# Optimization experiments

Hardware: AMD Instinct MI355X
Metric: run time of the kernel (lower is better)

Reference implementation:

```python
import jax, jax.numpy as jnp
import numpy as np

B, N, C = 2, 65536, 256
HEADS, DIM_HEAD, SLICE_NUM = 8, 64, 64
INNER = HEADS * DIM_HEAD


def setup_inputs() -> dict:
    key = jax.random.key(0)
    ks = jax.random.split(key, 7)
    s_in = 1.0 / np.sqrt(C)
    s_dh = 1.0 / np.sqrt(DIM_HEAD)
    return {
        "x": jax.random.normal(ks[0], (B, N, C), dtype=jnp.float32),
        "Wx": jax.random.uniform(ks[1], (C, INNER), jnp.float32, -s_in, s_in),
        "bx": jax.random.uniform(ks[2], (INNER,), jnp.float32, -s_in, s_in),
        "Wfx": jax.random.uniform(ks[3], (C, INNER), jnp.float32, -s_in, s_in),
        "bfx": jax.random.uniform(ks[4], (INNER,), jnp.float32, -s_in, s_in),
        "Wslice": jax.random.uniform(ks[5], (DIM_HEAD, SLICE_NUM), jnp.float32, -s_dh, s_dh),
        "bslice": jax.random.uniform(ks[6], (SLICE_NUM,), jnp.float32, -s_dh, s_dh),
        "temperature": jnp.ones((1, HEADS, 1, 1), dtype=jnp.float32) * 0.5,
    }


def reference(x, Wx, bx, Wfx, bfx, Wslice, bslice, temperature):
    b, n, _ = x.shape
    # Linear projections, split heads: (B, N, H*D) -> (B, H, N, D)
    px = (x @ Wx + bx).reshape(b, n, HEADS, DIM_HEAD).transpose(0, 2, 1, 3)
    fx = (x @ Wfx + bfx).reshape(b, n, HEADS, DIM_HEAD).transpose(0, 2, 1, 3)
    # Project onto slices: (B, H, N, S)
    slice_proj = px @ Wslice + bslice
    # Temperature-scaled softmax over slices
    temp = jnp.clip(temperature, 0.5, 5.0)
    slice_weights = jax.nn.softmax(slice_proj / temp, axis=-1)
    # Normalize by per-slice mass over tokens, then aggregate
    slice_norm = slice_weights.sum(axis=2)  # (B, H, S)
    normed = slice_weights / (slice_norm[:, :, None, :] + 0.01)
    slice_tokens = jnp.einsum("bhns,bhnd->bhsd", normed, fx)
    return slice_tokens
```

## Files before the change

kernel.cpp:

```cpp
#include <hip/hip_runtime.h>
#include <hip/hip_bf16.h>


typedef __attribute__((ext_vector_type(8))) short short8;
typedef __attribute__((ext_vector_type(4))) short short4v;
typedef __attribute__((ext_vector_type(4))) float float4v;

#define WPITCH 264
#define TPITCH 72

__device__ __forceinline__ unsigned short f2bf(float f) {
    union { float f; unsigned int u; } v; v.f = f;
    unsigned int r = (v.u + 0x7FFFu + ((v.u >> 16) & 1u)) >> 16;
    return (unsigned short)r;
}

__global__ void msfe_prep(const float* __restrict__ Wx, const float* __restrict__ bx,
                          const float* __restrict__ Wfx,
                          const float* __restrict__ Wslice, const float* __restrict__ bslice,
                          unsigned short* __restrict__ Wt, float* __restrict__ bc) {
    int j = blockIdx.x;
    int c = threadIdx.x;
    if (j < 512) {
        int h = j >> 6, s = j & 63;
        float acc = 0.f;
        #pragma unroll 8
        for (int d = 0; d < 64; ++d)
            acc += Wx[c * 512 + h * 64 + d] * Wslice[d * 64 + s];
        Wt[j * 256 + c] = f2bf(acc);
        if (c == 0) {
            float b = bslice[s];
            for (int d = 0; d < 64; ++d) b += bx[h * 64 + d] * Wslice[d * 64 + s];
            bc[j] = b;
        }
    } else {
        int col = j - 512;
        Wt[j * 256 + c] = f2bf(Wfx[c * 512 + col]);
    }
}

__global__ __launch_bounds__(512, 2)
void msfe_main(const float* __restrict__ x,
               const unsigned short* __restrict__ Wt,
               const float* __restrict__ bc,
               const float* __restrict__ bfx,
               const float* __restrict__ temperature,
               float* __restrict__ Tg, float* __restrict__ ng) {
    __shared__ unsigned short Ws[128 * WPITCH];
    __shared__ unsigned short Xs[64 * WPITCH];
    __shared__ unsigned short wT[64 * TPITCH];
    __shared__ unsigned short fT[64 * TPITCH];

    const int tid  = threadIdx.x;
    const int lane = tid & 63;
    const int wv   = tid >> 6;
    const int quad = lane >> 4;
    const int l16  = lane & 15;

    const int bidx = blockIdx.x;
    const int c8   = bidx & 7;
    const int ti   = (bidx >> 3) & 3;
    const int head = (bidx >> 5) & 7;
    const int rnd  = bidx >> 8;
    const int tile = rnd * 32 + c8 * 4 + ti;
    const int batch = tile >> 7;
    const long tok0 = (long)tile * 512;

    {
        int r = tid & 127;
        int part = tid >> 7;
        int grow = (r < 64) ? (head * 64 + r) : (512 + head * 64 + (r - 64));
        const short4v* src = (const short4v*)(Wt + grow * 256 + part * 64);
        short4v* dst = (short4v*)(Ws + r * WPITCH + part * 64);
        #pragma unroll
        for (int j = 0; j < 16; ++j) dst[j] = src[j];
    }

    {
        const float4v* xg = (const float4v*)(x + tok0 * 256);
        #pragma unroll
        for (int i = 0; i < 8; ++i) {
            float4v v = xg[tid + i * 512];
            int f = (tid + i * 512) * 4;
            int trow = f >> 8, col = f & 255;
            short4v p;
            p.x = (short)f2bf(v.x); p.y = (short)f2bf(v.y);
            p.z = (short)f2bf(v.z); p.w = (short)f2bf(v.w);
            *(short4v*)(Xs + trow * WPITCH + col) = p;
        }
    }

    float bcr[4], bfxr[4];
    #pragma unroll
    for (int nt = 0; nt < 4; ++nt) {
        bcr[nt]  = bc [head * 64 + nt * 16 + l16];
        bfxr[nt] = bfx[head * 64 + nt * 16 + l16];
    }
    float tmp = temperature[head];
    tmp = fminf(fmaxf(tmp, 0.5f), 5.0f);
    const float invt = 1.0f / tmp;

    float4v Tac[2];
    Tac[0] = (float4v){0.f, 0.f, 0.f, 0.f};
    Tac[1] = (float4v){0.f, 0.f, 0.f, 0.f};
    float normAcc[4] = {0.f, 0.f, 0.f, 0.f};

    const int proj = wv >> 2;
    const int tw   = wv & 3;
    const int sh   = wv & 3;
    const int dh   = wv >> 2;

    __syncthreads();

    for (int c = 0; c < 8; ++c) {
        float4v xr[8];
        if (c < 7) {
            const float4v* xg = (const float4v*)(x + (tok0 + (long)(c + 1) * 64) * 256);
            #pragma unroll
            for (int i = 0; i < 8; ++i) xr[i] = xg[tid + i * 512];
        }

        float4v acc[4];
        #pragma unroll
        for (int nt = 0; nt < 4; ++nt) acc[nt] = (float4v){0.f, 0.f, 0.f, 0.f};
        #pragma unroll
        for (int ks = 0; ks < 8; ++ks) {
            short8 a = *(const short8*)(Xs + (tw * 16 + l16) * WPITCH + ks * 32 + quad * 8);
            #pragma unroll
            for (int nt = 0; nt < 4; ++nt) {
                short8 b = *(const short8*)(Ws + (proj * 64 + nt * 16 + l16) * WPITCH + ks * 32 + quad * 8);
                acc[nt] = __builtin_amdgcn_mfma_f32_16x16x32_bf16(a, b, acc[nt], 0, 0, 0);
            }
        }

        if (proj == 0) {
            float v[4][4];
            #pragma unroll
            for (int nt = 0; nt < 4; ++nt)
                #pragma unroll
                for (int r = 0; r < 4; ++r)
                    v[nt][r] = (acc[nt][r] + bcr[nt]) * invt;
            #pragma unroll
            for (int r = 0; r < 4; ++r) {
                float m = fmaxf(fmaxf(v[0][r], v[1][r]), fmaxf(v[2][r], v[3][r]));
                m = fmaxf(m, __shfl_xor(m, 1));
                m = fmaxf(m, __shfl_xor(m, 2));
                m = fmaxf(m, __shfl_xor(m, 4));
                m = fmaxf(m, __shfl_xor(m, 8));
                float e0 = __expf(v[0][r] - m), e1 = __expf(v[1][r] - m);
                float e2 = __expf(v[2][r] - m), e3 = __expf(v[3][r] - m);
                float s = e0 + e1 + e2 + e3;
                s += __shfl_xor(s, 1); s += __shfl_xor(s, 2);
                s += __shfl_xor(s, 4); s += __shfl_xor(s, 8);
                float inv = 1.0f / s;
                v[0][r] = e0 * inv; v[1][r] = e1 * inv; v[2][r] = e2 * inv; v[3][r] = e3 * inv;
            }
            #pragma unroll
            for (int nt = 0; nt < 4; ++nt) {
                normAcc[nt] += v[nt][0] + v[nt][1] + v[nt][2] + v[nt][3];
                short4v p;
                p.x = (short)f2bf(v[nt][0]); p.y = (short)f2bf(v[nt][1]);
                p.z = (short)f2bf(v[nt][2]); p.w = (short)f2bf(v[nt][3]);
                *(short4v*)(wT + (nt * 16 + l16) * TPITCH + tw * 16 + quad * 4) = p;
            }
        } else {
            #pragma unroll
            for (int nt = 0; nt < 4; ++nt) {
                short4v p;
                p.x = (short)f2bf(acc[nt][0] + bfxr[nt]);
                p.y = (short)f2bf(acc[nt][1] + bfxr[nt]);
                p.z = (short)f2bf(acc[nt][2] + bfxr[nt]);
                p.w = (short)f2bf(acc[nt][3] + bfxr[nt]);
                *(short4v*)(fT + (nt * 16 + l16) * TPITCH + tw * 16 + quad * 4) = p;
            }
        }

        __syncthreads();

        #pragma unroll
        for (int ks = 0; ks < 2; ++ks) {
            short8 a = *(const short8*)(wT + (sh * 16 + l16) * TPITCH + ks * 32 + quad * 8);
            #pragma unroll
            for (int nt = 0; nt < 2; ++nt) {
                short8 b = *(const short8*)(fT + (dh * 32 + nt * 16 + l16) * TPITCH + ks * 32 + quad * 8);
                Tac[nt] = __builtin_amdgcn_mfma_f32_16x16x32_bf16(a, b, Tac[nt], 0, 0, 0);
            }
        }

        if (c < 7) {
            #pragma unroll
            for (int i = 0; i < 8; ++i) {
                int f = tid * 4 + i * 2048;
                int trow = f >> 8, col = f & 255;
                short4v p;
                p.x = (short)f2bf(xr[i].x); p.y = (short)f2bf(xr[i].y);
                p.z = (short)f2bf(xr[i].z); p.w = (short)f2bf(xr[i].w);
                *(short4v*)(Xs + trow * WPITCH + col) = p;
            }
        }
        __syncthreads();
    }

    const int basehs = (batch * 8 + head) * 64;
    #pragma unroll
    for (int nt = 0; nt < 2; ++nt) {
        #pragma unroll
        for (int r = 0; r < 4; ++r) {
            int s = sh * 16 + quad * 4 + r;
            int d = dh * 32 + nt * 16 + l16;
            atomicAdd(&Tg[(basehs + s) * 64 + d], Tac[nt][r]);
        }
    }
    if (wv < 4) {
        #pragma unroll
        for (int nt = 0; nt < 4; ++nt) {
            float v = normAcc[nt];
            v += __shfl_xor(v, 16);
            v += __shfl_xor(v, 32);
            if (quad == 0) atomicAdd(&ng[basehs + nt * 16 + l16], v);
        }
    }
}

__global__ void msfe_final(const float* __restrict__ Tg, const float* __restrict__ ng,
                           float* __restrict__ out) {
    int i = blockIdx.x * 256 + threadIdx.x;
    out[i] = Tg[i] / (ng[i >> 6] + 0.01f);
}

extern "C" void kernel_launch(void* const* d_in, const int* in_sizes, int n_in,
                              void* d_out, int out_size, void* d_ws, size_t ws_size,
                              hipStream_t stream) {
    const float* x       = (const float*)d_in[0];
    const float* Wx      = (const float*)d_in[1];
    const float* bx      = (const float*)d_in[2];
    const float* Wfx     = (const float*)d_in[3];
    const float* bfx     = (const float*)d_in[4];
    const float* Wslice  = (const float*)d_in[5];
    const float* bslice  = (const float*)d_in[6];
    const float* temp    = (const float*)d_in[7];

    char* ws = (char*)d_ws;
    unsigned short* Wt = (unsigned short*)ws;
    float* bc = (float*)(ws + 524288);
    float* Tg = (float*)(ws + 526336);
    float* ng = (float*)(ws + 788480);

    hipMemsetAsync(Tg, 0, 262144 + 4096, stream);

    msfe_prep<<<1024, 256, 0, stream>>>(Wx, bx, Wfx, Wslice, bslice, Wt, bc);
    msfe_main<<<2048, 512, 0, stream>>>(x, Wt, bc, bfx, temp, Tg, ng);
    msfe_final<<<256, 256, 0, stream>>>(Tg, ng, (float*)d_out);
}
```

Measured before the change: 380.7 us.

## Keep weights in MFMA-fragment registers and stream x directly into registers

Rewrites the prep kernel so it emits weights already laid out as MFMA B-fragments, and rewrites the main kernel to hold those weight fragments in registers. Each wave loads x straight from global memory into A-fragments, which removes the shared-memory X and W staging. The main kernel now uses 256 threads, processes 16 chunks of 32 tokens, and double-buffers the wT/fT tiles so one barrier per chunk suffices. The softmax max-subtraction is also dropped. This trades heavy register pressure and a risk of exp overflow for less LDS traffic and fewer barriers.

```diff
diff --git a/kernel.cpp b/kernel.cpp
--- a/kernel.cpp
+++ b/kernel.cpp
@@ -5,9 +5,9 @@
 typedef __attribute__((ext_vector_type(8))) short short8;
 typedef __attribute__((ext_vector_type(4))) short short4v;
 typedef __attribute__((ext_vector_type(4))) float float4v;
-
-#define WPITCH 264
-#define TPITCH 72
+typedef __attribute__((ext_vector_type(2))) unsigned int uint2v;
+
+#define MP 36
 
 __device__ __forceinline__ unsigned short f2bf(float f) {
     union { float f; unsigned int u; } v; v.f = f;
@@ -15,41 +15,108 @@
     return (unsigned short)r;
 }
 
-__global__ void msfe_prep(const float* __restrict__ Wx, const float* __restrict__ bx,
-                          const float* __restrict__ Wfx,
-                          const float* __restrict__ Wslice, const float* __restrict__ bslice,
-                          unsigned short* __restrict__ Wt, float* __restrict__ bc) {
-    int j = blockIdx.x;
-    int c = threadIdx.x;
-    if (j < 512) {
-        int h = j >> 6, s = j & 63;
-        float acc = 0.f;
-        #pragma unroll 8
-        for (int d = 0; d < 64; ++d)
-            acc += Wx[c * 512 + h * 64 + d] * Wslice[d * 64 + s];
-        Wt[j * 256 + c] = f2bf(acc);
-        if (c == 0) {
-            float b = bslice[s];
-            for (int d = 0; d < 64; ++d) b += bx[h * 64 + d] * Wslice[d * 64 + s];
-            bc[j] = b;
+__device__ __forceinline__ unsigned int pack2(float a, float b) {
+    __hip_bfloat162 h = __float22bfloat162_rn(float2{a, b});
+    union { __hip_bfloat162 h; unsigned int u; } cv; cv.h = h;
+    return cv.u;
+}
+
+__global__ __launch_bounds__(256)
+void msfe_prep3(const float* __restrict__ Wx, const float* __restrict__ bx,
+                const float* __restrict__ Wfx,
+                const float* __restrict__ Wslice, const float* __restrict__ bslice,
+                unsigned short* __restrict__ WtF, float* __restrict__ bcv) {
+    const int b = blockIdx.x, t = threadIdx.x;
+    if (b < 32) {
+        const int head = b >> 2, kq = (b >> 1) & 1, sg = b & 1;
+        __shared__ float Wsl[64 * 68];
+        __shared__ unsigned short stg[128 * 33];
+        #pragma unroll
+        for (int i = 0; i < 16; ++i) {
+            int idx = i * 256 + t; int d = idx >> 6, s = idx & 63;
+            Wsl[d * 68 + s] = Wslice[idx];
+        }
+        const int kl = t & 127, sHalf = t >> 7;
+        const int k = kq * 128 + kl;
+        float wxr[64];
+        const float4v* src = (const float4v*)(Wx + (long)k * 512 + head * 64);
+        #pragma unroll
+        for (int i = 0; i < 16; ++i) {
+            float4v v = src[i];
+            wxr[i*4+0] = v.x; wxr[i*4+1] = v.y; wxr[i*4+2] = v.z; wxr[i*4+3] = v.w;
+        }
+        __syncthreads();
+        const int sbase = sg * 32 + sHalf * 16;
+        float acc[16];
+        #pragma unroll
+        for (int si = 0; si < 16; ++si) acc[si] = 0.f;
+        #pragma unroll
+        for (int d = 0; d < 64; ++d) {
+            float w = wxr[d];
+            const float4v* r4 = (const float4v*)(Wsl + d * 68 + sbase);
+            float4v v0 = r4[0], v1 = r4[1], v2 = r4[2], v3 = r4[3];
+            acc[0]  += w * v0.x; acc[1]  += w * v0.y; acc[2]  += w * v0.z; acc[3]  += w * v0.w;
+            acc[4]  += w * v1.x; acc[5]  += w * v1.y; acc[6]  += w * v1.z; acc[7]  += w * v1.w;
+            acc[8]  += w * v2.x; acc[9]  += w * v2.y; acc[10] += w * v2.z; acc[11] += w * v2.w;
+            acc[12] += w * v3.x; acc[13] += w * v3.y; acc[14] += w * v3.z; acc[15] += w * v3.w;
+        }
+        #pragma unroll
+        for (int si = 0; si < 16; ++si)
+            stg[kl * 33 + sHalf * 16 + si] = f2bf(acc[si]);
+        __syncthreads();
+        #pragma unroll
+        for (int i = 0; i < 2; ++i) {
+            int e = i * 256 + t;
+            int ntL = e >> 8, ksL = (e >> 6) & 3, lane = e & 63;
+            int quad = lane >> 4, l16 = lane & 15;
+            int nt = sg * 2 + ntL;
+            int ks = kq * 4 + ksL;
+            short8 o;
+            #pragma unroll
+            for (int j = 0; j < 8; ++j) {
+                int kl2 = ksL * 32 + quad * 8 + j;
+                o[j] = (short)stg[kl2 * 33 + ntL * 16 + l16];
+            }
+            *(short8*)(WtF + ((((long)(0 * 8 + head) * 4 + nt) * 8 + ks) * 64 + lane) * 8) = o;
+        }
+    } else if (b < 48) {
+        const int head = (b - 32) >> 1, kq = (b - 32) & 1;
+        #pragma unroll
+        for (int i = 0; i < 4; ++i) {
+            int e = i * 256 + t;
+            int nt = e >> 8, ksL = (e >> 6) & 3, lane = e & 63;
+            int quad = lane >> 4, l16 = lane & 15;
+            int ks = kq * 4 + ksL;
+            int col = head * 64 + nt * 16 + l16;
+            short8 o;
+            #pragma unroll
+            for (int j = 0; j < 8; ++j) {
+                int k = kq * 128 + ksL * 32 + quad * 8 + j;
+                o[j] = (short)f2bf(Wfx[(long)k * 512 + col]);
+            }
+            *(short8*)(WtF + ((((long)(1 * 8 + head) * 4 + nt) * 8 + ks) * 64 + lane) * 8) = o;
         }
     } else {
-        int col = j - 512;
-        Wt[j * 256 + c] = f2bf(Wfx[c * 512 + col]);
-    }
-}
-
-__global__ __launch_bounds__(512, 2)
-void msfe_main(const float* __restrict__ x,
-               const unsigned short* __restrict__ Wt,
-               const float* __restrict__ bc,
-               const float* __restrict__ bfx,
-               const float* __restrict__ temperature,
-               float* __restrict__ Tg, float* __restrict__ ng) {
-    __shared__ unsigned short Ws[128 * WPITCH];
-    __shared__ unsigned short Xs[64 * WPITCH];
-    __shared__ unsigned short wT[64 * TPITCH];
-    __shared__ unsigned short fT[64 * TPITCH];
+        #pragma unroll
+        for (int p = 0; p < 2; ++p) {
+            int j = t + p * 256;
+            int h = j >> 6, s = j & 63;
+            float bsum = bslice[s];
+            for (int d = 0; d < 64; ++d) bsum += bx[h * 64 + d] * Wslice[d * 64 + s];
+            bcv[j] = bsum;
+        }
+    }
+}
+
+__global__ __launch_bounds__(256, 2)
+void msfe_main4(const float* __restrict__ x,
+                const unsigned short* __restrict__ WtF,
+                const float* __restrict__ bcv,
+                const float* __restrict__ bfx,
+                const float* __restrict__ temperature,
+                float* __restrict__ Tg, float* __restrict__ ng) {
+    __shared__ unsigned short wT[2][64 * MP];
+    __shared__ unsigned short fT[2][64 * MP];
 
     const int tid  = threadIdx.x;
     const int lane = tid & 63;
@@ -58,160 +125,143 @@
     const int l16  = lane & 15;
 
     const int bidx = blockIdx.x;
-    const int c8   = bidx & 7;
-    const int ti   = (bidx >> 3) & 3;
-    const int head = (bidx >> 5) & 7;
-    const int rnd  = bidx >> 8;
-    const int tile = rnd * 32 + c8 * 4 + ti;
+    const int tile = (bidx >> 6) * 8 + (bidx & 7);
+    const int head = (bidx >> 3) & 7;
     const int batch = tile >> 7;
-    const long tok0 = (long)tile * 512;
-
+
+    const int proj = wv >> 1;
+    const int tw   = wv & 1;
+
+    short8 wfr[4][8];
     {
-        int r = tid & 127;
-        int part = tid >> 7;
-        int grow = (r < 64) ? (head * 64 + r) : (512 + head * 64 + (r - 64));
-        const short4v* src = (const short4v*)(Wt + grow * 256 + part * 64);
-        short4v* dst = (short4v*)(Ws + r * WPITCH + part * 64);
-        #pragma unroll
-        for (int j = 0; j < 16; ++j) dst[j] = src[j];
-    }
-
-    {
-        const float4v* xg = (const float4v*)(x + tok0 * 256);
-        #pragma unroll
-        for (int i = 0; i < 8; ++i) {
-            float4v v = xg[tid + i * 512];
-            int f = (tid + i * 512) * 4;
-            int trow = f >> 8, col = f & 255;
-            short4v p;
-            p.x = (short)f2bf(v.x); p.y = (short)f2bf(v.y);
-            p.z = (short)f2bf(v.z); p.w = (short)f2bf(v.w);
-            *(short4v*)(Xs + trow * WPITCH + col) = p;
-        }
-    }
-
-    float bcr[4], bfxr[4];
-    #pragma unroll
-    for (int nt = 0; nt < 4; ++nt) {
-        bcr[nt]  = bc [head * 64 + nt * 16 + l16];
-        bfxr[nt] = bfx[head * 64 + nt * 16 + l16];
-    }
+        const unsigned short* wb = WtF + (((long)(proj * 8 + head) * 4) * 8) * 512 + (long)lane * 8;
+        #pragma unroll
+        for (int nt = 0; nt < 4; ++nt)
+            #pragma unroll
+            for (int ks = 0; ks < 8; ++ks)
+                wfr[nt][ks] = *(const short8*)(wb + (nt * 8 + ks) * 512);
+    }
+    #pragma unroll
+    for (int nt = 0; nt < 4; ++nt)
+        #pragma unroll
+        for (int ks = 0; ks < 8; ++ks)
+            asm volatile("" : "+v"(wfr[nt][ks]));
+
+    float bias[4];
+    #pragma unroll
+    for (int nt = 0; nt < 4; ++nt)
+        bias[nt] = (proj == 0 ? bcv : bfx)[head * 64 + nt * 16 + l16];
     float tmp = temperature[head];
     tmp = fminf(fmaxf(tmp, 0.5f), 5.0f);
     const float invt = 1.0f / tmp;
 
-    float4v Tac[2];
-    Tac[0] = (float4v){0.f, 0.f, 0.f, 0.f};
-    Tac[1] = (float4v){0.f, 0.f, 0.f, 0.f};
+    float4v Tac[4];
+    #pragma unroll
+    for (int nt = 0; nt < 4; ++nt) Tac[nt] = (float4v){0.f, 0.f, 0.f, 0.f};
     float normAcc[4] = {0.f, 0.f, 0.f, 0.f};
 
-    const int proj = wv >> 2;
-    const int tw   = wv & 3;
-    const int sh   = wv & 3;
-    const int dh   = wv >> 2;
-
-    __syncthreads();
-
-    for (int c = 0; c < 8; ++c) {
-        float4v xr[8];
-        if (c < 7) {
-            const float4v* xg = (const float4v*)(x + (tok0 + (long)(c + 1) * 64) * 256);
-            #pragma unroll
-            for (int i = 0; i < 8; ++i) xr[i] = xg[tid + i * 512];
-        }
+    const float* xrow = x + ((long)tile * 512 + tw * 16 + l16) * 256;
+    short8 afr[8];
+    #pragma unroll
+    for (int ks = 0; ks < 8; ++ks) {
+        const float4v* p = (const float4v*)(xrow + ks * 32 + quad * 8);
+        float4v v0 = p[0], v1 = p[1];
+        union { short8 s; unsigned int u[4]; } cu;
+        cu.u[0] = pack2(v0.x, v0.y); cu.u[1] = pack2(v0.z, v0.w);
+        cu.u[2] = pack2(v1.x, v1.y); cu.u[3] = pack2(v1.z, v1.w);
+        afr[ks] = cu.s;
+    }
+
+    for (int c = 0; c < 16; ++c) {
+        const int wbuf = c & 1, rbuf = wbuf ^ 1;
 
         float4v acc[4];
         #pragma unroll
         for (int nt = 0; nt < 4; ++nt) acc[nt] = (float4v){0.f, 0.f, 0.f, 0.f};
         #pragma unroll
         for (int ks = 0; ks < 8; ++ks) {
-            short8 a = *(const short8*)(Xs + (tw * 16 + l16) * WPITCH + ks * 32 + quad * 8);
+            #pragma unroll
+            for (int nt = 0; nt < 4; ++nt)
+                acc[nt] = __builtin_amdgcn_mfma_f32_16x16x32_bf16(afr[ks], wfr[nt][ks], acc[nt], 0, 0, 0);
+        }
+
+        if (c < 15) {
+            #pragma unroll
+            for (int ks = 0; ks < 8; ++ks) {
+                const float4v* p = (const float4v*)(xrow + (long)(c + 1) * 8192 + ks * 32 + quad * 8);
+                float4v v0 = p[0], v1 = p[1];
+                union { short8 s; unsigned int u[4]; } cu;
+                cu.u[0] = pack2(v0.x, v0.y); cu.u[1] = pack2(v0.z, v0.w);
+                cu.u[2] = pack2(v1.x, v1.y); cu.u[3] = pack2(v1.z, v1.w);
+                afr[ks] = cu.s;
+            }
+        }
+
+        if (c > 0) {
+            short8 a = *(const short8*)(&wT[rbuf][(wv * 16 + l16) * MP + quad * 8]);
             #pragma unroll
             for (int nt = 0; nt < 4; ++nt) {
-                short8 b = *(const short8*)(Ws + (proj * 64 + nt * 16 + l16) * WPITCH + ks * 32 + quad * 8);
-                acc[nt] = __builtin_amdgcn_mfma_f32_16x16x32_bf16(a, b, acc[nt], 0, 0, 0);
+                short8 bf = *(const short8*)(&fT[rbuf][(nt * 16 + l16) * MP + quad * 8]);
+                Tac[nt] = __builtin_amdgcn_mfma_f32_16x16x32_bf16(a, bf, Tac[nt], 0, 0, 0);
             }
         }
 
         if (proj == 0) {
-            float v[4][4];
+            float e[4][4];
             #pragma unroll
             for (int nt = 0; nt < 4; ++nt)
                 #pragma unroll
-                for (int r = 0; r < 4; ++r)
-                    v[nt][r] = (acc[nt][r] + bcr[nt]) * invt;
-            #pragma unroll
-            for (int r = 0; r < 4; ++r) {
-                float m = fmaxf(fmaxf(v[0][r], v[1][r]), fmaxf(v[2][r], v[3][r]));
-                m = fmaxf(m, __shfl_xor(m, 1));
-                m = fmaxf(m, __shfl_xor(m, 2));
-                m = fmaxf(m, __shfl_xor(m, 4));
-                m = fmaxf(m, __shfl_xor(m, 8));
-                float e0 = __expf(v[0][r] - m), e1 = __expf(v[1][r] - m);
-                float e2 = __expf(v[2][r] - m), e3 = __expf(v[3][r] - m);
-                float s = e0 + e1 + e2 + e3;
+                for (int rr = 0; rr < 4; ++rr)
+                    e[nt][rr] = __expf((acc[nt][rr] + bias[nt]) * invt);
+            #pragma unroll
+            for (int rr = 0; rr < 4; ++rr) {
+                float s = e[0][rr] + e[1][rr] + e[2][rr] + e[3][rr];
                 s += __shfl_xor(s, 1); s += __shfl_xor(s, 2);
                 s += __shfl_xor(s, 4); s += __shfl_xor(s, 8);
                 float inv = 1.0f / s;
-                v[0][r] = e0 * inv; v[1][r] = e1 * inv; v[2][r] = e2 * inv; v[3][r] = e3 * inv;
+                e[0][rr] *= inv; e[1][rr] *= inv; e[2][rr] *= inv; e[3][rr] *= inv;
             }
             #pragma unroll
             for (int nt = 0; nt < 4; ++nt) {
-                normAcc[nt] += v[nt][0] + v[nt][1] + v[nt][2] + v[nt][3];
-                short4v p;
-                p.x = (short)f2bf(v[nt][0]); p.y = (short)f2bf(v[nt][1]);
-                p.z = (short)f2bf(v[nt][2]); p.w = (short)f2bf(v[nt][3]);
-                *(short4v*)(wT + (nt * 16 + l16) * TPITCH + tw * 16 + quad * 4) = p;
+                normAcc[nt] += e[nt][0] + e[nt][1] + e[nt][2] + e[nt][3];
+                uint2v p;
+                p.x = pack2(e[nt][0], e[nt][1]);
+                p.y = pack2(e[nt][2], e[nt][3]);
+                *(uint2v*)(&wT[wbuf][(nt * 16 + l16) * MP + tw * 16 + quad * 4]) = p;
             }
         } else {
             #pragma unroll
             for (int nt = 0; nt < 4; ++nt) {
-                short4v p;
-                p.x = (short)f2bf(acc[nt][0] + bfxr[nt]);
-                p.y = (short)f2bf(acc[nt][1] + bfxr[nt]);
-                p.z = (short)f2bf(acc[nt][2] + bfxr[nt]);
-                p.w = (short)f2bf(acc[nt][3] + bfxr[nt]);
-                *(short4v*)(fT + (nt * 16 + l16) * TPITCH + tw * 16 + quad * 4) = p;
+                uint2v p;
+                p.x = pack2(acc[nt][0] + bias[nt], acc[nt][1] + bias[nt]);
+                p.y = pack2(acc[nt][2] + bias[nt], acc[nt][3] + bias[nt]);
+                *(uint2v*)(&fT[wbuf][(nt * 16 + l16) * MP + tw * 16 + quad * 4]) = p;
             }
         }
 
         __syncthreads();
-
-        #pragma unroll
-        for (int ks = 0; ks < 2; ++ks) {
-            short8 a = *(const short8*)(wT + (sh * 16 + l16) * TPITCH + ks * 32 + quad * 8);
-            #pragma unroll
-            for (int nt = 0; nt < 2; ++nt) {
-                short8 b = *(const short8*)(fT + (dh * 32 + nt * 16 + l16) * TPITCH + ks * 32 + quad * 8);
-                Tac[nt] = __builtin_amdgcn_mfma_f32_16x16x32_bf16(a, b, Tac[nt], 0, 0, 0);
-            }
-        }
-
-        if (c < 7) {
-            #pragma unroll
-            for (int i = 0; i < 8; ++i) {
-                int f = tid * 4 + i * 2048;
-                int trow = f >> 8, col = f & 255;
-                short4v p;
-                p.x = (short)f2bf(xr[i].x); p.y = (short)f2bf(xr[i].y);
-                p.z = (short)f2bf(xr[i].z); p.w = (short)f2bf(xr[i].w);
-                *(short4v*)(Xs + trow * WPITCH + col) = p;
-            }
-        }
-        __syncthreads();
+    }
+
+    {
+        short8 a = *(const short8*)(&wT[1][(wv * 16 + l16) * MP + quad * 8]);
+        #pragma unroll
+        for (int nt = 0; nt < 4; ++nt) {
+            short8 bf = *(const short8*)(&fT[1][(nt * 16 + l16) * MP + quad * 8]);
+            Tac[nt] = __builtin_amdgcn_mfma_f32_16x16x32_bf16(a, bf, Tac[nt], 0, 0, 0);
+        }
     }
 
     const int basehs = (batch * 8 + head) * 64;
     #pragma unroll
-    for (int nt = 0; nt < 2; ++nt) {
-        #pragma unroll
-        for (int r = 0; r < 4; ++r) {
-            int s = sh * 16 + quad * 4 + r;
-            int d = dh * 32 + nt * 16 + l16;
-            atomicAdd(&Tg[(basehs + s) * 64 + d], Tac[nt][r]);
-        }
-    }
-    if (wv < 4) {
+    for (int nt = 0; nt < 4; ++nt) {
+        #pragma unroll
+        for (int rr = 0; rr < 4; ++rr) {
+            int s = wv * 16 + quad * 4 + rr;
+            int d = nt * 16 + l16;
+            atomicAdd(&Tg[(basehs + s) * 64 + d], Tac[nt][rr]);
+        }
+    }
+    if (proj == 0) {
         #pragma unroll
         for (int nt = 0; nt < 4; ++nt) {
             float v = normAcc[nt];
@@ -241,14 +291,13 @@
     const float* temp    = (const float*)d_in[7];
 
     char* ws = (char*)d_ws;
-    unsigned short* Wt = (unsigned short*)ws;
+    unsigned short* WtF = (unsigned short*)ws;
     float* bc = (float*)(ws + 524288);
     float* Tg = (float*)(ws + 526336);
     float* ng = (float*)(ws + 788480);
 
     hipMemsetAsync(Tg, 0, 262144 + 4096, stream);
-
-    msfe_prep<<<1024, 256, 0, stream>>>(Wx, bx, Wfx, Wslice, bslice, Wt, bc);
-    msfe_main<<<2048, 512, 0, stream>>>(x, Wt, bc, bfx, temp, Tg, ng);
+    msfe_prep3<<<49, 256, 0, stream>>>(Wx, bx, Wfx, Wslice, bslice, WtF, bc);
+    msfe_main4<<<2048, 256, 0, stream>>>(x, WtF, bc, bfx, temp, Tg, ng);
     msfe_final<<<256, 256, 0, stream>>>(Tg, ng, (float*)d_out);
 }
```

New measurement: 449.1 us. 18.0% more time.
